# Kernel tuning notes

Hardware: AMD Instinct MI355X
Metric: run time of the kernel (lower is better)

Reference implementation:

```python
import jax, jax.numpy as jnp
import numpy as np

EPS = 0.0  # original torch code has no eps; exact division by L2 norm

def setup_inputs() -> dict:
    key = jax.random.key(0)
    k1, k2 = jax.random.split(key)
    N, D = 262144, 256
    query_emb = jax.random.normal(k1, (N, D), dtype=jnp.float32)
    doc_emb = jax.random.normal(k2, (N, D), dtype=jnp.float32)
    return {"query_emb": query_emb, "doc_emb": doc_emb}

def reference(query_emb, doc_emb):
    # L2-normalize rows, then per-row dot product.
    # Mathematically identical to diag(qn @ dn.T) in the torch module,
    # but computed in O(N*d) instead of materializing an NxN matrix.
    q_norm = jnp.linalg.norm(query_emb, axis=1, keepdims=True)
    d_norm = jnp.linalg.norm(doc_emb, axis=1, keepdims=True)
    qn = query_emb / q_norm
    dn = doc_emb / d_norm
    sim_score = jnp.sum(qn * dn, axis=1, keepdims=True)  # [N, 1]
    return sim_score
```

## Files before the change

kernel.cpp:

```cpp
#include <hip/hip_runtime.h>

typedef float fx4 __attribute__((ext_vector_type(4)));
typedef float fx2 __attribute__((ext_vector_type(2)));

constexpr int ROWS_PER_WAVE = 2;

__global__ __launch_bounds__(256) void cosine_rows_kernel(
    const fx4* __restrict__ q4,
    const fx4* __restrict__ d4,
    fx2* __restrict__ out2,
    int n_rows)
{
    const int wave = (blockIdx.x * blockDim.x + threadIdx.x) >> 6;
    const int lane = threadIdx.x & 63;
    const int row0 = wave * ROWS_PER_WAVE;
    if (row0 >= n_rows) return;

    fx4 qv[ROWS_PER_WAVE], dv[ROWS_PER_WAVE];
    #pragma unroll
    for (int r = 0; r < ROWS_PER_WAVE; ++r) {
        const size_t base = (size_t)(row0 + r) * 64 + lane;
        qv[r] = __builtin_nontemporal_load(&q4[base]);
        dv[r] = __builtin_nontemporal_load(&d4[base]);
    }

    float res[ROWS_PER_WAVE];
    #pragma unroll
    for (int r = 0; r < ROWS_PER_WAVE; ++r) {
        float qq = qv[r].x * qv[r].x + qv[r].y * qv[r].y +
                   qv[r].z * qv[r].z + qv[r].w * qv[r].w;
        float dd = dv[r].x * dv[r].x + dv[r].y * dv[r].y +
                   dv[r].z * dv[r].z + dv[r].w * dv[r].w;
        float qd = qv[r].x * dv[r].x + qv[r].y * dv[r].y +
                   qv[r].z * dv[r].z + qv[r].w * dv[r].w;

        #pragma unroll
        for (int off = 32; off > 0; off >>= 1) {
            qq += __shfl_xor(qq, off, 64);
            dd += __shfl_xor(dd, off, 64);
            qd += __shfl_xor(qd, off, 64);
        }
        res[r] = qd * rsqrtf(qq * dd);
    }

    if (lane == 0) {
        fx2 o;
        o.x = res[0];
        o.y = res[1];
        __builtin_nontemporal_store(o, &out2[wave]);
    }
}

extern "C" void kernel_launch(void* const* d_in, const int* in_sizes, int n_in,
                              void* d_out, int out_size, void* d_ws, size_t ws_size,
                              hipStream_t stream) {
    const fx4* q4 = (const fx4*)d_in[0];
    const fx4* d4 = (const fx4*)d_in[1];
    fx2* out2 = (fx2*)d_out;

    const int D = 256;
    const int n_rows = in_sizes[0] / D;

    const int rows_per_block = 4 * ROWS_PER_WAVE;
    const int grid = (n_rows + rows_per_block - 1) / rows_per_block;

    cosine_rows_kernel<<<grid, 256, 0, stream>>>(q4, d4, out2, n_rows);
}
```

Before: 466.9 us.

## Map 16 lanes per row with four rows per wave and more loads in flight

```diff
diff --git a/kernel.cpp b/kernel.cpp
--- a/kernel.cpp
+++ b/kernel.cpp
@@ -1,53 +1,53 @@
 #include <hip/hip_runtime.h>
 
 typedef float fx4 __attribute__((ext_vector_type(4)));
-typedef float fx2 __attribute__((ext_vector_type(2)));
 
-constexpr int ROWS_PER_WAVE = 2;
+constexpr int ROWS_PER_WAVE = 4;
+constexpr int WAVES_PER_BLOCK = 4;
 
 __global__ __launch_bounds__(256) void cosine_rows_kernel(
     const fx4* __restrict__ q4,
     const fx4* __restrict__ d4,
-    fx2* __restrict__ out2,
+    float* __restrict__ out,
     int n_rows)
 {
     const int wave = (blockIdx.x * blockDim.x + threadIdx.x) >> 6;
     const int lane = threadIdx.x & 63;
-    const int row0 = wave * ROWS_PER_WAVE;
-    if (row0 >= n_rows) return;
+    const int g    = lane >> 4;
+    const int c    = lane & 15;
+    const int row  = wave * ROWS_PER_WAVE + g;
+    if (row >= n_rows) return;
 
-    fx4 qv[ROWS_PER_WAVE], dv[ROWS_PER_WAVE];
+    const size_t base = (size_t)row * 64 + c;
+
+    fx4 qv[4], dv[4];
     #pragma unroll
-    for (int r = 0; r < ROWS_PER_WAVE; ++r) {
-        const size_t base = (size_t)(row0 + r) * 64 + lane;
-        qv[r] = __builtin_nontemporal_load(&q4[base]);
-        dv[r] = __builtin_nontemporal_load(&d4[base]);
+    for (int k = 0; k < 4; ++k)
+        qv[k] = __builtin_nontemporal_load(&q4[base + 16 * k]);
+    #pragma unroll
+    for (int k = 0; k < 4; ++k)
+        dv[k] = __builtin_nontemporal_load(&d4[base + 16 * k]);
+
+    float qq = 0.0f, dd = 0.0f, qd = 0.0f;
+    #pragma unroll
+    for (int k = 0; k < 4; ++k) {
+        qq += qv[k].x * qv[k].x + qv[k].y * qv[k].y +
+              qv[k].z * qv[k].z + qv[k].w * qv[k].w;
+        dd += dv[k].x * dv[k].x + dv[k].y * dv[k].y +
+              dv[k].z * dv[k].z + dv[k].w * dv[k].w;
+        qd += qv[k].x * dv[k].x + qv[k].y * dv[k].y +
+              qv[k].z * dv[k].z + qv[k].w * dv[k].w;
     }
 
-    float res[ROWS_PER_WAVE];
     #pragma unroll
-    for (int r = 0; r < ROWS_PER_WAVE; ++r) {
-        float qq = qv[r].x * qv[r].x + qv[r].y * qv[r].y +
-                   qv[r].z * qv[r].z + qv[r].w * qv[r].w;
-        float dd = dv[r].x * dv[r].x + dv[r].y * dv[r].y +
-                   dv[r].z * dv[r].z + dv[r].w * dv[r].w;
-        float qd = qv[r].x * dv[r].x + qv[r].y * dv[r].y +
-                   qv[r].z * dv[r].z + qv[r].w * dv[r].w;
-
-        #pragma unroll
-        for (int off = 32; off > 0; off >>= 1) {
-            qq += __shfl_xor(qq, off, 64);
-            dd += __shfl_xor(dd, off, 64);
-            qd += __shfl_xor(qd, off, 64);
-        }
-        res[r] = qd * rsqrtf(qq * dd);
+    for (int off = 8; off > 0; off >>= 1) {
+        qq += __shfl_xor(qq, off, 64);
+        dd += __shfl_xor(dd, off, 64);
+        qd += __shfl_xor(qd, off, 64);
     }
 
-    if (lane == 0) {
-        fx2 o;
-        o.x = res[0];
-        o.y = res[1];
-        __builtin_nontemporal_store(o, &out2[wave]);
+    if (c == 0) {
+        __builtin_nontemporal_store(qd * rsqrtf(qq * dd), &out[row]);
     }
 }
 
@@ -56,13 +56,13 @@
                               hipStream_t stream) {
     const fx4* q4 = (const fx4*)d_in[0];
     const fx4* d4 = (const fx4*)d_in[1];
-    fx2* out2 = (fx2*)d_out;
+    float* out = (float*)d_out;
 
     const int D = 256;
     const int n_rows = in_sizes[0] / D;
 
-    const int rows_per_block = 4 * ROWS_PER_WAVE;
+    const int rows_per_block = WAVES_PER_BLOCK * ROWS_PER_WAVE;
     const int grid = (n_rows + rows_per_block - 1) / rows_per_block;
 
-    cosine_rows_kernel<<<grid, 256, 0, stream>>>(q4, d4, out2, n_rows);
+    cosine_rows_kernel<<<grid, 256, 0, stream>>>(q4, d4, out, n_rows);
 }
```

Result: no change. 465.9 us (-0.2%).
